# Optimization experiments

Measured on AMD Instinct MI355X. Metric: run time of the kernel, lower is better.

## Reference

```python
import jax, jax.numpy as jnp
import numpy as np
import hashlib

VOCAB = 50257
EMBED_DIM = 1024
STEPS = 8
B, L = 8, 8192


def _build_c_table(vocab: int) -> np.ndarray:
    # Precompute the SHA256-derived complex constant c for every token id.
    # Matches: real = int(h[:16],16)/2**64 - 0.5 ; imag = int(h[16:32],16)/2**64 - 0.5 ; *2.0
    tbl = np.empty((vocab, 2), dtype=np.float32)
    for tid in range(vocab):
        h = hashlib.sha256(str(tid).encode()).hexdigest()
        tbl[tid, 0] = (int(h[:16], 16) / 2**64 - 0.5) * 2.0
        tbl[tid, 1] = (int(h[16:32], 16) / 2**64 - 0.5) * 2.0
    return tbl


def setup_inputs() -> dict:
    key = jax.random.key(0)
    k1, k2 = jax.random.split(key)
    token_ids = jax.random.randint(k1, (B, L), 0, VOCAB, dtype=jnp.int64 if jax.config.jax_enable_x64 else jnp.int32)
    c_table = jnp.asarray(_build_c_table(VOCAB))                      # (V, 2)
    # nn.Linear(2*steps, embed_dim, bias=False): weight shape (embed_dim, 2*steps)
    W = jax.random.normal(k2, (EMBED_DIM, 2 * STEPS), dtype=jnp.float32) * (1.0 / np.sqrt(2 * STEPS))
    scale = jnp.ones((), dtype=jnp.float32)
    return {"token_ids": token_ids, "c_table": c_table, "W": W, "scale": scale}


def _julia_features(token_ids, c_table, steps):
    c = c_table[token_ids]                 # (B, L, 2) gather
    cr, ci = c[..., 0], c[..., 1]
    zr = jnp.zeros_like(cr)
    zi = jnp.zeros_like(ci)
    feats = []
    for _ in range(steps):                 # fixed small unrolled recurrence
        zr, zi = zr * zr - zi * zi + cr, 2.0 * zr * zi + ci
        feats.append(zr)
        feats.append(zi)
    # interleaved [zr_0, zi_0, zr_1, zi_1, ...] == torch.cat of (...,2) blocks
    return jnp.stack(feats, axis=-1)       # (B, L, 2*steps)


def reference(token_ids, c_table, W, scale):
    steps = W.shape[1] // 2
    feats = _julia_features(token_ids, c_table, steps)   # (B, L, 2*steps)
    out = jnp.einsum('blf,df->bld', feats, W) * scale    # (B, L, embed_dim)
    return out
```

## Files before the change

kernel.cpp:

```cpp
#include <hip/hip_runtime.h>


#define STEPS 8
#define NFEAT (2 * STEPS)
#define EMBED 1024
#define NTOK (8 * 8192)
#define NPAIR (NTOK / 2)
#define BLOCK 256
#define GRID 2048

typedef float floatx4 __attribute__((ext_vector_type(4)));

__global__ __launch_bounds__(BLOCK, 4) void FractalEmbedding_30365418782757_kernel(
    const int* __restrict__ tok,
    const float* __restrict__ ctab,
    const float* __restrict__ W,
    const float* __restrict__ scale_p,
    float* __restrict__ out)
{
    const int t = threadIdx.x;
    const float s = *scale_p;

    float w[4][NFEAT];
#pragma unroll
    for (int r = 0; r < 4; ++r) {
        const float4* wrow = reinterpret_cast<const float4*>(W + (size_t)(4 * t + r) * NFEAT);
#pragma unroll
        for (int q = 0; q < 4; ++q) {
            float4 v = wrow[q];
            w[r][4 * q + 0] = v.x * s;
            w[r][4 * q + 1] = v.y * s;
            w[r][4 * q + 2] = v.z * s;
            w[r][4 * q + 3] = v.w * s;
        }
    }

    const int2*   tok2  = reinterpret_cast<const int2*>(tok);
    const float2* ctab2 = reinterpret_cast<const float2*>(ctab);

    int p = blockIdx.x;
    int2   id = tok2[p];
    float2 c0 = ctab2[id.x];
    float2 c1 = ctab2[id.y];

    for (; p < NPAIR; p += GRID) {
        const int pn = p + GRID;
        const int pc = (pn < NPAIR) ? pn : p;
        int2   idn = tok2[pc];
        float2 cn0 = ctab2[idn.x];
        float2 cn1 = ctab2[idn.y];

        float acc0[4] = {0.f, 0.f, 0.f, 0.f};
        float acc1[4] = {0.f, 0.f, 0.f, 0.f};
        float zr0 = 0.f, zi0 = 0.f, zr1 = 0.f, zi1 = 0.f;
#pragma unroll
        for (int st = 0; st < STEPS; ++st) {
            float a0 = zr0 * zr0 - zi0 * zi0 + c0.x;
            float b0 = 2.0f * zr0 * zi0 + c0.y;
            zr0 = a0; zi0 = b0;
            float a1 = zr1 * zr1 - zi1 * zi1 + c1.x;
            float b1 = 2.0f * zr1 * zi1 + c1.y;
            zr1 = a1; zi1 = b1;
#pragma unroll
            for (int r = 0; r < 4; ++r) {
                acc0[r] += zr0 * w[r][2 * st];
                acc0[r] += zi0 * w[r][2 * st + 1];
                acc1[r] += zr1 * w[r][2 * st];
                acc1[r] += zi1 * w[r][2 * st + 1];
            }
        }

        floatx4 o0 = {acc0[0], acc0[1], acc0[2], acc0[3]};
        floatx4 o1 = {acc1[0], acc1[1], acc1[2], acc1[3]};
        __builtin_nontemporal_store(o0, reinterpret_cast<floatx4*>(out + (size_t)(2 * p)     * EMBED) + t);
        __builtin_nontemporal_store(o1, reinterpret_cast<floatx4*>(out + (size_t)(2 * p + 1) * EMBED) + t);

        c0 = cn0;
        c1 = cn1;
    }
}

extern "C" void kernel_launch(void* const* d_in, const int* in_sizes, int n_in,
                              void* d_out, int out_size, void* d_ws, size_t ws_size,
                              hipStream_t stream) {
    const int*   tok   = (const int*)d_in[0];
    const float* ctab  = (const float*)d_in[1];
    const float* W     = (const float*)d_in[2];
    const float* scale = (const float*)d_in[3];
    float*       out   = (float*)d_out;

    FractalEmbedding_30365418782757_kernel<<<GRID, BLOCK, 0, stream>>>(tok, ctab, W, scale, out);
}
```

Measured before the change: 57.89 us.

## Assign contiguous token tiles per block with shared-memory staged hash constants

```diff
diff --git a/kernel.cpp b/kernel.cpp
--- a/kernel.cpp
+++ b/kernel.cpp
@@ -5,11 +5,9 @@
 #define NFEAT (2 * STEPS)
 #define EMBED 1024
 #define NTOK (8 * 8192)
-#define NPAIR (NTOK / 2)
+#define TPB 64
 #define BLOCK 256
-#define GRID 2048
-
-typedef float floatx4 __attribute__((ext_vector_type(4)));
+#define GRID (NTOK / TPB)
 
 __global__ __launch_bounds__(BLOCK, 4) void FractalEmbedding_30365418782757_kernel(
     const int* __restrict__ tok,
@@ -20,6 +18,14 @@
 {
     const int t = threadIdx.x;
     const float s = *scale_p;
+
+    __shared__ float2 cs[TPB];
+
+    const int base = blockIdx.x * TPB;
+    if (t < TPB) {
+        const int id = tok[base + t];
+        cs[t] = reinterpret_cast<const float2*>(ctab)[id];
+    }
 
     float w[4][NFEAT];
 #pragma unroll
@@ -35,32 +41,27 @@
         }
     }
 
-    const int2*   tok2  = reinterpret_cast<const int2*>(tok);
-    const float2* ctab2 = reinterpret_cast<const float2*>(ctab);
+    __syncthreads();
 
-    int p = blockIdx.x;
-    int2   id = tok2[p];
-    float2 c0 = ctab2[id.x];
-    float2 c1 = ctab2[id.y];
-
-    for (; p < NPAIR; p += GRID) {
-        const int pn = p + GRID;
-        const int pc = (pn < NPAIR) ? pn : p;
-        int2   idn = tok2[pc];
-        float2 cn0 = ctab2[idn.x];
-        float2 cn1 = ctab2[idn.y];
+    float2 c0 = cs[0];
+    float2 c1 = cs[1];
+#pragma unroll 1
+    for (int i = 0; i < TPB; i += 2) {
+        const int nn = (i + 2 < TPB) ? (i + 2) : i;
+        float2 cn0 = cs[nn];
+        float2 cn1 = cs[nn + 1];
 
         float acc0[4] = {0.f, 0.f, 0.f, 0.f};
         float acc1[4] = {0.f, 0.f, 0.f, 0.f};
         float zr0 = 0.f, zi0 = 0.f, zr1 = 0.f, zi1 = 0.f;
 #pragma unroll
         for (int st = 0; st < STEPS; ++st) {
-            float a0 = zr0 * zr0 - zi0 * zi0 + c0.x;
-            float b0 = 2.0f * zr0 * zi0 + c0.y;
-            zr0 = a0; zi0 = b0;
-            float a1 = zr1 * zr1 - zi1 * zi1 + c1.x;
-            float b1 = 2.0f * zr1 * zi1 + c1.y;
-            zr1 = a1; zi1 = b1;
+            float x0 = zr0 * zr0 - zi0 * zi0 + c0.x;
+            float y0 = 2.0f * zr0 * zi0 + c0.y;
+            zr0 = x0; zi0 = y0;
+            float x1 = zr1 * zr1 - zi1 * zi1 + c1.x;
+            float y1 = 2.0f * zr1 * zi1 + c1.y;
+            zr1 = x1; zi1 = y1;
 #pragma unroll
             for (int r = 0; r < 4; ++r) {
                 acc0[r] += zr0 * w[r][2 * st];
@@ -70,10 +71,10 @@
             }
         }
 
-        floatx4 o0 = {acc0[0], acc0[1], acc0[2], acc0[3]};
-        floatx4 o1 = {acc1[0], acc1[1], acc1[2], acc1[3]};
-        __builtin_nontemporal_store(o0, reinterpret_cast<floatx4*>(out + (size_t)(2 * p)     * EMBED) + t);
-        __builtin_nontemporal_store(o1, reinterpret_cast<floatx4*>(out + (size_t)(2 * p + 1) * EMBED) + t);
+        float4 o0; o0.x = acc0[0]; o0.y = acc0[1]; o0.z = acc0[2]; o0.w = acc0[3];
+        float4 o1; o1.x = acc1[0]; o1.y = acc1[1]; o1.z = acc1[2]; o1.w = acc1[3];
+        reinterpret_cast<float4*>(out + (size_t)(base + i)     * EMBED)[t] = o0;
+        reinterpret_cast<float4*>(out + (size_t)(base + i + 1) * EMBED)[t] = o1;
 
         c0 = cn0;
         c1 = cn1;
```

New measurement: 55.25 us. 4.6% less time.
